# Kernel optimization log

Hardware: AMD Instinct MI355X
Metric: run time of the kernel (lower is better)

Reference implementation:

```python
import jax, jax.numpy as jnp
import numpy as np

N = 100000
D = 16          # input_dim
NUM_FILTERS = 8
NNZ = 1600000


def setup_inputs() -> dict:
    key = jax.random.key(0)
    k1, k2, k3, k4, k5 = jax.random.split(key, 5)
    x = jax.random.normal(k1, (N, D), dtype=jnp.float32)
    L_rows = jax.random.randint(k2, (NNZ,), 0, N, dtype=jnp.int64 if jax.config.jax_enable_x64 else jnp.int32).astype(jnp.int32)
    L_cols = jax.random.randint(k3, (NNZ,), 0, N, dtype=jnp.int32)
    L_v = jax.random.normal(k4, (NNZ,), dtype=jnp.float32)
    node_attr_eig = jax.random.uniform(k5, (N,), dtype=jnp.float32)
    return {"x": x, "L_rows": L_rows, "L_cols": L_cols, "L_v": L_v, "node_attr_eig": node_attr_eig}


def reference(x, L_rows, L_cols, L_v, node_attr_eig):
    n, d = x.shape
    f = NUM_FILTERS
    # exponents = 2 ** arange(num_filters + 1)
    exponents = (2 ** jnp.arange(f + 1)).astype(x.dtype)  # [F+1]
    # coeffs = x.T @ L  ==  (L.T @ x).T ; compute L.T @ x as [N, D]
    # (L.T @ x)[c] = sum over nnz entries (r, c): L_v * x[r]
    LTx = jax.ops.segment_sum(L_v[:, None] * x[L_rows], L_cols, num_segments=n)  # [N, D]
    # exponential eigenfilter bank: w = exp(-eig)^exponents, wavelet differences
    w = jnp.exp(-node_attr_eig)[:, None] ** exponents[None, :]  # [N, F+1]
    w_wav = w[:, :-1] - w[:, 1:]                                # [N, F]
    # g_eig = coeffs[..., None] * w_wav[None, ...] permuted to [N, D, F]
    g_eig = (LTx[:, :, None] * w_wav[:, None, :]).reshape(n, d * f)  # [N, D*F]
    # filtered = L @ g_eig : out[r] = sum over nnz (r, c): L_v * g_eig[c]
    out = jax.ops.segment_sum(L_v[:, None] * g_eig[L_cols], L_rows, num_segments=n)
    return out.reshape(n, d, f)
```

## Files before the change

kernel.cpp:

```cpp
#include <hip/hip_runtime.h>

#define N_NODES   100000
#define D_DIM     16
#define NFILT     8
#define KOUT      128
#define NNZ_CNT   1600000

#define SHIFT1    12
#define NC1       25
#define CAP1      67072
#define NSUB      32
#define CROWS     128
#define NCB       (NC1 * NSUB)
#define CAP       2560
#define EPB       2048
#define NBLKA     ((NNZ_CNT + EPB - 1) / EPB)
#define CHB       ((CAP1 + EPB - 1) / EPB)
#define CPAD      16

__device__ __forceinline__ uint f32_to_bf16_bits(float f) {
    uint u = __float_as_uint(f);
    uint r = (u + 0x7FFFu + ((u >> 16) & 1u)) >> 16;
    return r;
}

__global__ void wav_kernel(const float* __restrict__ eig, ushort* __restrict__ wavb) {
    int n = blockIdx.x * blockDim.x + threadIdx.x;
    if (n >= N_NODES) return;
    float cur = expf(-eig[n]);
    uint pk[4];
#pragma unroll
    for (int h = 0; h < 4; ++h) {
        float nx0 = cur * cur;
        float w0 = cur - nx0;
        float nx1 = nx0 * nx0;
        float w1 = nx0 - nx1;
        cur = nx1;
        pk[h] = f32_to_bf16_bits(w0) | (f32_to_bf16_bits(w1) << 16);
    }
    *(uint4*)(wavb + (size_t)n * NFILT) = make_uint4(pk[0], pk[1], pk[2], pk[3]);
}

__global__ __launch_bounds__(512) void binC_kernel(const int* __restrict__ keys,
                                                   const int* __restrict__ pays,
                                                   const float* __restrict__ v,
                                                   int* __restrict__ gcur1,
                                                   int2* __restrict__ regB) {
    __shared__ int cnt[NC1], offb[NC1], gbase[NC1], cur[NC1];
    __shared__ int2 rec[EPB];
    __shared__ unsigned char rbk[EPB];
    int tid = threadIdx.x;
    int e0 = blockIdx.x * EPB;
    int nE = NNZ_CNT - e0; if (nE > EPB) nE = EPB;

    if (tid < NC1) cnt[tid] = 0;
    __syncthreads();

    int k_[4], p_[4], vb_[4];
    int nk = 0;
#pragma unroll
    for (int kk = 0; kk < 4; ++kk) {
        int i = tid + kk * 512;
        if (i < nE) {
            k_[kk] = keys[e0 + i];
            p_[kk] = pays[e0 + i];
            vb_[kk] = __float_as_int(v[e0 + i]);
            nk = kk + 1;
            atomicAdd(&cnt[k_[kk] >> SHIFT1], 1);
        }
    }
    __syncthreads();

    if (tid == 0) {
        int run = 0;
        for (int b = 0; b < NC1; ++b) { offb[b] = run; run += cnt[b]; }
    }
    if (tid < NC1)
        gbase[tid] = cnt[tid] ? atomicAdd(&gcur1[tid * CPAD], cnt[tid]) : 0;
    __syncthreads();
    if (tid < NC1) cur[tid] = offb[tid];
    __syncthreads();

    for (int kk = 0; kk < nk; ++kk) {
        int b = k_[kk] >> SHIFT1;
        int pos = atomicAdd(&cur[b], 1);
        rec[pos] = make_int2(((k_[kk] & ((1 << SHIFT1) - 1)) << 17) | p_[kk], vb_[kk]);
        rbk[pos] = (unsigned char)b;
    }
    __syncthreads();

    for (int i = tid; i < nE; i += 512) {
        int b = rbk[i];
        int slot = gbase[b] + (i - offb[b]);
        if (slot < CAP1) regB[(size_t)b * CAP1 + slot] = rec[i];
    }
}

__global__ __launch_bounds__(512) void binF_kernel(const int* __restrict__ gcur1,
                                                   const int2* __restrict__ regB,
                                                   int* __restrict__ gcurF,
                                                   int2* __restrict__ regA) {
    __shared__ int cnt[NSUB], offb[NSUB], gbase[NSUB], cur[NSUB];
    __shared__ int2 rec[EPB];
    __shared__ unsigned char rbk[EPB];
    int tid = threadIdx.x;
    int cb = blockIdx.x / CHB;
    int ch = blockIdx.x % CHB;
    int nc = gcur1[cb * CPAD]; if (nc > CAP1) nc = CAP1;
    int cs = ch * EPB;
    if (cs >= nc) return;
    int nE = nc - cs; if (nE > EPB) nE = EPB;
    size_t srcb = (size_t)cb * CAP1 + cs;

    if (tid < NSUB) cnt[tid] = 0;
    __syncthreads();

    int2 my[4]; int msub[4];
    int nk = 0;
#pragma unroll
    for (int kk = 0; kk < 4; ++kk) {
        int i = tid + kk * 512;
        msub[kk] = -1;
        if (i < nE) {
            my[kk] = regB[srcb + i];
            msub[kk] = (my[kk].x >> 24) & (NSUB - 1);
            nk = kk + 1;
            atomicAdd(&cnt[msub[kk]], 1);
        }
    }
    __syncthreads();

    if (tid == 0) {
        int run = 0;
        for (int b = 0; b < NSUB; ++b) { offb[b] = run; run += cnt[b]; }
    }
    if (tid < NSUB)
        gbase[tid] = cnt[tid] ? atomicAdd(&gcurF[(cb * NSUB + tid) * CPAD], cnt[tid]) : 0;
    __syncthreads();
    if (tid < NSUB) cur[tid] = offb[tid];
    __syncthreads();

    for (int kk = 0; kk < nk; ++kk)
        if (msub[kk] >= 0) {
            int pos = atomicAdd(&cur[msub[kk]], 1);
            rec[pos] = make_int2(my[kk].x & 0xFFFFFF, my[kk].y);
            rbk[pos] = (unsigned char)msub[kk];
        }
    __syncthreads();

    for (int i = tid; i < nE; i += 512) {
        int b = rbk[i];
        int slot = gbase[b] + (i - offb[b]);
        if (slot < CAP)
            regA[(size_t)(cb * NSUB + b) * CAP + slot] = rec[i];
    }
}

__global__ __launch_bounds__(512) void sortgather1_kernel(const int* __restrict__ gcurF,
                                                          const int2* __restrict__ regA,
                                                          const float* __restrict__ x,
                                                          uint* __restrict__ LTxP) {
    __shared__ int2 rec[CAP];
    __shared__ int cnt[CROWS];
    __shared__ int sc[CROWS];
    __shared__ int st[CROWS];
    __shared__ int cur[CROWS];
    int tid = threadIdx.x;
    int b = blockIdx.x;
    int nb = gcurF[b * CPAD]; if (nb > CAP) nb = CAP;
    size_t base = (size_t)b * CAP;

    int2 my[5]; int mkey[5];
    if (tid < CROWS) cnt[tid] = 0;
    __syncthreads();
#pragma unroll
    for (int s = 0; s < 5; ++s) {
        int i = tid + s * 512;
        mkey[s] = -1;
        if (i < nb) {
            my[s] = regA[base + i];
            mkey[s] = my[s].x >> 17;
            atomicAdd(&cnt[mkey[s]], 1);
        }
    }
    __syncthreads();

    int cv = (tid < CROWS) ? cnt[tid] : 0;
    if (tid < CROWS) sc[tid] = cv;
    __syncthreads();
    for (int off = 1; off < CROWS; off <<= 1) {
        int t = (tid < CROWS && tid >= off) ? sc[tid - off] : 0;
        __syncthreads();
        if (tid < CROWS) sc[tid] += t;
        __syncthreads();
    }
    if (tid < CROWS) { int s0 = sc[tid] - cv; st[tid] = s0; cur[tid] = s0; }
    __syncthreads();

#pragma unroll
    for (int s = 0; s < 5; ++s)
        if (mkey[s] >= 0) {
            int pos = atomicAdd(&cur[mkey[s]], 1);
            if (pos < CAP) rec[pos] = make_int2(my[s].x & 0x1FFFF, my[s].y);
        }
    __syncthreads();

    int wave = tid >> 6, lane = tid & 63;
    int d = lane & 15, j = lane >> 4;
    for (int cl = wave; cl < CROWS; cl += 8) {
        int c = b * CROWS + cl;
        int i0 = st[cl], e0 = i0 + cnt[cl]; if (e0 > CAP) e0 = CAP;
        float acc = 0.f;
        for (int i = i0 + j; i < e0; i += 4) {
            int2 e = rec[i];
            acc = fmaf(__int_as_float(e.y), x[(size_t)e.x * D_DIM + d], acc);
        }
        acc += __shfl_xor(acc, 16);
        acc += __shfl_xor(acc, 32);
        float hi = __shfl_down(acc, 8);
        if (lane < 8 && c < N_NODES)
            LTxP[(size_t)c * NFILT + lane] =
                f32_to_bf16_bits(acc) | (f32_to_bf16_bits(hi) << 16);
    }
}

__global__ __launch_bounds__(512) void sortgather2_kernel(const int* __restrict__ gcurF,
                                                          const int2* __restrict__ regA,
                                                          const uint* __restrict__ LTxP,
                                                          const ushort* __restrict__ wavb,
                                                          float* __restrict__ out) {
    __shared__ int2 rec[CAP];
    __shared__ int cnt[CROWS];
    __shared__ int sc[CROWS];
    __shared__ int st[CROWS];
    __shared__ int cur[CROWS];
    int tid = threadIdx.x;
    int b = blockIdx.x;
    int nb = gcurF[b * CPAD]; if (nb > CAP) nb = CAP;
    size_t base = (size_t)b * CAP;

    int2 my[5]; int mkey[5];
    if (tid < CROWS) cnt[tid] = 0;
    __syncthreads();
#pragma unroll
    for (int s = 0; s < 5; ++s) {
        int i = tid + s * 512;
        mkey[s] = -1;
        if (i < nb) {
            my[s] = regA[base + i];
            mkey[s] = my[s].x >> 17;
            atomicAdd(&cnt[mkey[s]], 1);
        }
    }
    __syncthreads();

    int cv = (tid < CROWS) ? cnt[tid] : 0;
    if (tid < CROWS) sc[tid] = cv;
    __syncthreads();
    for (int off = 1; off < CROWS; off <<= 1) {
        int t = (tid < CROWS && tid >= off) ? sc[tid - off] : 0;
        __syncthreads();
        if (tid < CROWS) sc[tid] += t;
        __syncthreads();
    }
    if (tid < CROWS) { int s0 = sc[tid] - cv; st[tid] = s0; cur[tid] = s0; }
    __syncthreads();

#pragma unroll
    for (int s = 0; s < 5; ++s)
        if (mkey[s] >= 0) {
            int pos = atomicAdd(&cur[mkey[s]], 1);
            if (pos < CAP) rec[pos] = make_int2(my[s].x & 0x1FFFF, my[s].y);
        }
    __syncthreads();

    int wave = tid >> 6, lane = tid & 63;
    int d0 = lane >> 3;
    int f  = lane & 7;
    for (int rl = wave; rl < CROWS; rl += 8) {
        int row = b * CROWS + rl;
        if (row >= N_NODES) continue;
        int i = st[rl], end = st[rl] + cnt[rl]; if (end > CAP) end = CAP;
        float acc0 = 0.f, acc1 = 0.f;
        for (; i + 4 <= end; i += 4) {
            int2 e0 = rec[i], e1 = rec[i + 1], e2 = rec[i + 2], e3 = rec[i + 3];
            uint l0 = LTxP[e0.x * NFILT + d0];
            uint l1 = LTxP[e1.x * NFILT + d0];
            uint l2 = LTxP[e2.x * NFILT + d0];
            uint l3 = LTxP[e3.x * NFILT + d0];
            uint w0 = wavb[e0.x * NFILT + f];
            uint w1 = wavb[e1.x * NFILT + f];
            uint w2 = wavb[e2.x * NFILT + f];
            uint w3 = wavb[e3.x * NFILT + f];
            float vw0 = __int_as_float(e0.y) * __uint_as_float(w0 << 16);
            float vw1 = __int_as_float(e1.y) * __uint_as_float(w1 << 16);
            float vw2 = __int_as_float(e2.y) * __uint_as_float(w2 << 16);
            float vw3 = __int_as_float(e3.y) * __uint_as_float(w3 << 16);
            acc0 = fmaf(vw0, __uint_as_float(l0 << 16), acc0);
            acc1 = fmaf(vw0, __uint_as_float(l0 & 0xFFFF0000u), acc1);
            acc0 = fmaf(vw1, __uint_as_float(l1 << 16), acc0);
            acc1 = fmaf(vw1, __uint_as_float(l1 & 0xFFFF0000u), acc1);
            acc0 = fmaf(vw2, __uint_as_float(l2 << 16), acc0);
            acc1 = fmaf(vw2, __uint_as_float(l2 & 0xFFFF0000u), acc1);
            acc0 = fmaf(vw3, __uint_as_float(l3 << 16), acc0);
            acc1 = fmaf(vw3, __uint_as_float(l3 & 0xFFFF0000u), acc1);
        }
        for (; i < end; ++i) {
            int2 e = rec[i];
            uint l = LTxP[e.x * NFILT + d0];
            uint w = wavb[e.x * NFILT + f];
            float vw = __int_as_float(e.y) * __uint_as_float(w << 16);
            acc0 = fmaf(vw, __uint_as_float(l << 16), acc0);
            acc1 = fmaf(vw, __uint_as_float(l & 0xFFFF0000u), acc1);
        }
        __builtin_nontemporal_store(acc0, &out[(size_t)row * KOUT + lane]);
        __builtin_nontemporal_store(acc1, &out[(size_t)row * KOUT + 64 + lane]);
    }
}

extern "C" void kernel_launch(void* const* d_in, const int* in_sizes, int n_in,
                              void* d_out, int out_size, void* d_ws, size_t ws_size,
                              hipStream_t stream) {
    const float* x      = (const float*)d_in[0];
    const int*   L_rows = (const int*)  d_in[1];
    const int*   L_cols = (const int*)  d_in[2];
    const float* L_v    = (const float*)d_in[3];
    const float* eig    = (const float*)d_in[4];
    float* out = (float*)d_out;

    uint*   LTxP = (uint*)d_ws;
    ushort* wavb = (ushort*)(LTxP + (size_t)N_NODES * NFILT);
    int2*   regB = (int2*)(wavb + (size_t)N_NODES * NFILT);
    int2*   regA = regB + (size_t)NC1 * CAP1;
    int*    gc1c = (int*)(regA + (size_t)NCB * CAP);
    int*    gc1r = gc1c + NC1 * CPAD;
    int*    gfc  = gc1r + NC1 * CPAD;
    int*    gfr  = gfc + NCB * CPAD;

    hipMemsetAsync(gc1c, 0, (size_t)(2 * NC1 + 2 * NCB) * CPAD * sizeof(int), stream);

    wav_kernel<<<(N_NODES + 255) / 256, 256, 0, stream>>>(eig, wavb);

    binC_kernel<<<NBLKA, 512, 0, stream>>>(L_cols, L_rows, L_v, gc1c, regB);
    binF_kernel<<<NC1 * CHB, 512, 0, stream>>>(gc1c, regB, gfc, regA);
    sortgather1_kernel<<<NCB, 512, 0, stream>>>(gfc, regA, x, LTxP);

    binC_kernel<<<NBLKA, 512, 0, stream>>>(L_rows, L_cols, L_v, gc1r, regB);
    binF_kernel<<<NC1 * CHB, 512, 0, stream>>>(gc1r, regB, gfr, regA);
    sortgather2_kernel<<<NCB, 512, 0, stream>>>(gfr, regA, LTxP, wavb, out);
}
```

Baseline: 277.9 us.

## Fuse both coarse binning passes, interleave LTx with wavelets, use finer row buckets

Merges the two coarse binning launches into one kernel that reads rows, cols and values once and scatters into separate column and row regions, removing a second pass over the COO inputs. LTx and wavelet weights are stored interleaved in one 64-byte record per node, so the second gather touches one cache line per neighbour instead of two. Buckets shrink to 64 rows with 256-thread blocks and a smaller capacity, doubling block count for better load balance. The risks are extra workspace for a second coarse region and a tighter per-bucket capacity that could overflow on skewed inputs.

```diff
diff --git a/kernel.cpp b/kernel.cpp
--- a/kernel.cpp
+++ b/kernel.cpp
@@ -9,22 +9,23 @@
 #define SHIFT1    12
 #define NC1       25
 #define CAP1      67072
-#define NSUB      32
-#define CROWS     128
+#define NSUB      64
+#define CROWS     64
 #define NCB       (NC1 * NSUB)
-#define CAP       2560
+#define CAP       1408
 #define EPB       2048
 #define NBLKA     ((NNZ_CNT + EPB - 1) / EPB)
 #define CHB       ((CAP1 + EPB - 1) / EPB)
 #define CPAD      16
 
+
 __device__ __forceinline__ uint f32_to_bf16_bits(float f) {
     uint u = __float_as_uint(f);
     uint r = (u + 0x7FFFu + ((u >> 16) & 1u)) >> 16;
     return r;
 }
 
-__global__ void wav_kernel(const float* __restrict__ eig, ushort* __restrict__ wavb) {
+__global__ void wav_kernel(const float* __restrict__ eig, uint* __restrict__ combo) {
     int n = blockIdx.x * blockDim.x + threadIdx.x;
     if (n >= N_NODES) return;
     float cur = expf(-eig[n]);
@@ -38,14 +39,16 @@
         cur = nx1;
         pk[h] = f32_to_bf16_bits(w0) | (f32_to_bf16_bits(w1) << 16);
     }
-    *(uint4*)(wavb + (size_t)n * NFILT) = make_uint4(pk[0], pk[1], pk[2], pk[3]);
-}
-
-__global__ __launch_bounds__(512) void binC_kernel(const int* __restrict__ keys,
-                                                   const int* __restrict__ pays,
-                                                   const float* __restrict__ v,
-                                                   int* __restrict__ gcur1,
-                                                   int2* __restrict__ regB) {
+    *(uint4*)(combo + (size_t)n * 16 + 8) = make_uint4(pk[0], pk[1], pk[2], pk[3]);
+}
+
+__global__ __launch_bounds__(512) void binC2_kernel(const int* __restrict__ rows,
+                                                    const int* __restrict__ cols,
+                                                    const float* __restrict__ v,
+                                                    int* __restrict__ gc1c,
+                                                    int* __restrict__ gc1r,
+                                                    int2* __restrict__ regBc,
+                                                    int2* __restrict__ regBr) {
     __shared__ int cnt[NC1], offb[NC1], gbase[NC1], cur[NC1];
     __shared__ int2 rec[EPB];
     __shared__ unsigned char rbk[EPB];
@@ -53,46 +56,66 @@
     int e0 = blockIdx.x * EPB;
     int nE = NNZ_CNT - e0; if (nE > EPB) nE = EPB;
 
-    if (tid < NC1) cnt[tid] = 0;
-    __syncthreads();
-
-    int k_[4], p_[4], vb_[4];
+    int r_[4], c_[4], vb_[4];
     int nk = 0;
 #pragma unroll
     for (int kk = 0; kk < 4; ++kk) {
         int i = tid + kk * 512;
         if (i < nE) {
-            k_[kk] = keys[e0 + i];
-            p_[kk] = pays[e0 + i];
+            r_[kk] = rows[e0 + i];
+            c_[kk] = cols[e0 + i];
             vb_[kk] = __float_as_int(v[e0 + i]);
             nk = kk + 1;
-            atomicAdd(&cnt[k_[kk] >> SHIFT1], 1);
-        }
-    }
-    __syncthreads();
-
-    if (tid == 0) {
-        int run = 0;
-        for (int b = 0; b < NC1; ++b) { offb[b] = run; run += cnt[b]; }
-    }
-    if (tid < NC1)
-        gbase[tid] = cnt[tid] ? atomicAdd(&gcur1[tid * CPAD], cnt[tid]) : 0;
-    __syncthreads();
-    if (tid < NC1) cur[tid] = offb[tid];
-    __syncthreads();
-
+        }
+    }
+
+    if (tid < NC1) cnt[tid] = 0;
+    __syncthreads();
+    for (int kk = 0; kk < nk; ++kk) atomicAdd(&cnt[c_[kk] >> SHIFT1], 1);
+    __syncthreads();
+    if (tid == 0) { int run = 0; for (int b = 0; b < NC1; ++b) { offb[b] = run; run += cnt[b]; } }
+    __syncthreads();
+    if (tid < NC1) {
+        gbase[tid] = cnt[tid] ? atomicAdd(&gc1c[tid * CPAD], cnt[tid]) : 0;
+        cur[tid] = offb[tid];
+    }
+    __syncthreads();
     for (int kk = 0; kk < nk; ++kk) {
-        int b = k_[kk] >> SHIFT1;
+        int b = c_[kk] >> SHIFT1;
         int pos = atomicAdd(&cur[b], 1);
-        rec[pos] = make_int2(((k_[kk] & ((1 << SHIFT1) - 1)) << 17) | p_[kk], vb_[kk]);
+        rec[pos] = make_int2(((c_[kk] & 4095) << 17) | r_[kk], vb_[kk]);
         rbk[pos] = (unsigned char)b;
     }
     __syncthreads();
-
     for (int i = tid; i < nE; i += 512) {
         int b = rbk[i];
         int slot = gbase[b] + (i - offb[b]);
-        if (slot < CAP1) regB[(size_t)b * CAP1 + slot] = rec[i];
+        if (slot < CAP1) regBc[(size_t)b * CAP1 + slot] = rec[i];
+    }
+    __syncthreads();
+
+    if (tid < NC1) cnt[tid] = 0;
+    __syncthreads();
+    for (int kk = 0; kk < nk; ++kk) atomicAdd(&cnt[r_[kk] >> SHIFT1], 1);
+    __syncthreads();
+    if (tid == 0) { int run = 0; for (int b = 0; b < NC1; ++b) { offb[b] = run; run += cnt[b]; } }
+    __syncthreads();
+    if (tid < NC1) {
+        gbase[tid] = cnt[tid] ? atomicAdd(&gc1r[tid * CPAD], cnt[tid]) : 0;
+        cur[tid] = offb[tid];
+    }
+    __syncthreads();
+    for (int kk = 0; kk < nk; ++kk) {
+        int b = r_[kk] >> SHIFT1;
+        int pos = atomicAdd(&cur[b], 1);
+        rec[pos] = make_int2(((r_[kk] & 4095) << 17) | c_[kk], vb_[kk]);
+        rbk[pos] = (unsigned char)b;
+    }
+    __syncthreads();
+    for (int i = tid; i < nE; i += 512) {
+        int b = rbk[i];
+        int slot = gbase[b] + (i - offb[b]);
+        if (slot < CAP1) regBr[(size_t)b * CAP1 + slot] = rec[i];
     }
 }
 
@@ -123,27 +146,25 @@
         msub[kk] = -1;
         if (i < nE) {
             my[kk] = regB[srcb + i];
-            msub[kk] = (my[kk].x >> 24) & (NSUB - 1);
+            msub[kk] = (my[kk].x >> 23) & (NSUB - 1);
             nk = kk + 1;
             atomicAdd(&cnt[msub[kk]], 1);
         }
     }
     __syncthreads();
 
-    if (tid == 0) {
-        int run = 0;
-        for (int b = 0; b < NSUB; ++b) { offb[b] = run; run += cnt[b]; }
-    }
-    if (tid < NSUB)
+    if (tid == 0) { int run = 0; for (int b = 0; b < NSUB; ++b) { offb[b] = run; run += cnt[b]; } }
+    __syncthreads();
+    if (tid < NSUB) {
         gbase[tid] = cnt[tid] ? atomicAdd(&gcurF[(cb * NSUB + tid) * CPAD], cnt[tid]) : 0;
-    __syncthreads();
-    if (tid < NSUB) cur[tid] = offb[tid];
+        cur[tid] = offb[tid];
+    }
     __syncthreads();
 
     for (int kk = 0; kk < nk; ++kk)
         if (msub[kk] >= 0) {
             int pos = atomicAdd(&cur[msub[kk]], 1);
-            rec[pos] = make_int2(my[kk].x & 0xFFFFFF, my[kk].y);
+            rec[pos] = make_int2(my[kk].x & 0x7FFFFF, my[kk].y);
             rbk[pos] = (unsigned char)msub[kk];
         }
     __syncthreads();
@@ -156,26 +177,23 @@
     }
 }
 
-__global__ __launch_bounds__(512) void sortgather1_kernel(const int* __restrict__ gcurF,
+__global__ __launch_bounds__(256) void sortgather1_kernel(const int* __restrict__ gcurF,
                                                           const int2* __restrict__ regA,
                                                           const float* __restrict__ x,
-                                                          uint* __restrict__ LTxP) {
+                                                          uint* __restrict__ combo) {
     __shared__ int2 rec[CAP];
-    __shared__ int cnt[CROWS];
-    __shared__ int sc[CROWS];
-    __shared__ int st[CROWS];
-    __shared__ int cur[CROWS];
+    __shared__ int cnt[CROWS], sc[CROWS], st[CROWS], cur[CROWS];
     int tid = threadIdx.x;
     int b = blockIdx.x;
     int nb = gcurF[b * CPAD]; if (nb > CAP) nb = CAP;
     size_t base = (size_t)b * CAP;
 
-    int2 my[5]; int mkey[5];
+    int2 my[6]; int mkey[6];
     if (tid < CROWS) cnt[tid] = 0;
     __syncthreads();
 #pragma unroll
-    for (int s = 0; s < 5; ++s) {
-        int i = tid + s * 512;
+    for (int s = 0; s < 6; ++s) {
+        int i = tid + s * 256;
         mkey[s] = -1;
         if (i < nb) {
             my[s] = regA[base + i];
@@ -198,7 +216,7 @@
     __syncthreads();
 
 #pragma unroll
-    for (int s = 0; s < 5; ++s)
+    for (int s = 0; s < 6; ++s)
         if (mkey[s] >= 0) {
             int pos = atomicAdd(&cur[mkey[s]], 1);
             if (pos < CAP) rec[pos] = make_int2(my[s].x & 0x1FFFF, my[s].y);
@@ -207,7 +225,7 @@
 
     int wave = tid >> 6, lane = tid & 63;
     int d = lane & 15, j = lane >> 4;
-    for (int cl = wave; cl < CROWS; cl += 8) {
+    for (int cl = wave; cl < CROWS; cl += 4) {
         int c = b * CROWS + cl;
         int i0 = st[cl], e0 = i0 + cnt[cl]; if (e0 > CAP) e0 = CAP;
         float acc = 0.f;
@@ -219,32 +237,28 @@
         acc += __shfl_xor(acc, 32);
         float hi = __shfl_down(acc, 8);
         if (lane < 8 && c < N_NODES)
-            LTxP[(size_t)c * NFILT + lane] =
+            combo[(size_t)c * 16 + lane] =
                 f32_to_bf16_bits(acc) | (f32_to_bf16_bits(hi) << 16);
     }
 }
 
-__global__ __launch_bounds__(512) void sortgather2_kernel(const int* __restrict__ gcurF,
+__global__ __launch_bounds__(256) void sortgather2_kernel(const int* __restrict__ gcurF,
                                                           const int2* __restrict__ regA,
-                                                          const uint* __restrict__ LTxP,
-                                                          const ushort* __restrict__ wavb,
+                                                          const uint* __restrict__ combo,
                                                           float* __restrict__ out) {
     __shared__ int2 rec[CAP];
-    __shared__ int cnt[CROWS];
-    __shared__ int sc[CROWS];
-    __shared__ int st[CROWS];
-    __shared__ int cur[CROWS];
+    __shared__ int cnt[CROWS], sc[CROWS], st[CROWS], cur[CROWS];
     int tid = threadIdx.x;
     int b = blockIdx.x;
     int nb = gcurF[b * CPAD]; if (nb > CAP) nb = CAP;
     size_t base = (size_t)b * CAP;
 
-    int2 my[5]; int mkey[5];
+    int2 my[6]; int mkey[6];
     if (tid < CROWS) cnt[tid] = 0;
     __syncthreads();
 #pragma unroll
-    for (int s = 0; s < 5; ++s) {
-        int i = tid + s * 512;
+    for (int s = 0; s < 6; ++s) {
+        int i = tid + s * 256;
         mkey[s] = -1;
         if (i < nb) {
             my[s] = regA[base + i];
@@ -267,7 +281,7 @@
     __syncthreads();
 
 #pragma unroll
-    for (int s = 0; s < 5; ++s)
+    for (int s = 0; s < 6; ++s)
         if (mkey[s] >= 0) {
             int pos = atomicAdd(&cur[mkey[s]], 1);
             if (pos < CAP) rec[pos] = make_int2(my[s].x & 0x1FFFF, my[s].y);
@@ -277,21 +291,21 @@
     int wave = tid >> 6, lane = tid & 63;
     int d0 = lane >> 3;
     int f  = lane & 7;
-    for (int rl = wave; rl < CROWS; rl += 8) {
+    for (int rl = wave; rl < CROWS; rl += 4) {
         int row = b * CROWS + rl;
         if (row >= N_NODES) continue;
         int i = st[rl], end = st[rl] + cnt[rl]; if (end > CAP) end = CAP;
         float acc0 = 0.f, acc1 = 0.f;
         for (; i + 4 <= end; i += 4) {
             int2 e0 = rec[i], e1 = rec[i + 1], e2 = rec[i + 2], e3 = rec[i + 3];
-            uint l0 = LTxP[e0.x * NFILT + d0];
-            uint l1 = LTxP[e1.x * NFILT + d0];
-            uint l2 = LTxP[e2.x * NFILT + d0];
-            uint l3 = LTxP[e3.x * NFILT + d0];
-            uint w0 = wavb[e0.x * NFILT + f];
-            uint w1 = wavb[e1.x * NFILT + f];
-            uint w2 = wavb[e2.x * NFILT + f];
-            uint w3 = wavb[e3.x * NFILT + f];
+            uint l0 = combo[(size_t)e0.x * 16 + d0];
+            uint l1 = combo[(size_t)e1.x * 16 + d0];
+            uint l2 = combo[(size_t)e2.x * 16 + d0];
+            uint l3 = combo[(size_t)e3.x * 16 + d0];
+            uint w0 = ((const ushort*)(combo + (size_t)e0.x * 16 + 8))[f];
+            uint w1 = ((const ushort*)(combo + (size_t)e1.x * 16 + 8))[f];
+            uint w2 = ((const ushort*)(combo + (size_t)e2.x * 16 + 8))[f];
+            uint w3 = ((const ushort*)(combo + (size_t)e3.x * 16 + 8))[f];
             float vw0 = __int_as_float(e0.y) * __uint_as_float(w0 << 16);
             float vw1 = __int_as_float(e1.y) * __uint_as_float(w1 << 16);
             float vw2 = __int_as_float(e2.y) * __uint_as_float(w2 << 16);
@@ -307,8 +321,8 @@
         }
         for (; i < end; ++i) {
             int2 e = rec[i];
-            uint l = LTxP[e.x * NFILT + d0];
-            uint w = wavb[e.x * NFILT + f];
+            uint l = combo[(size_t)e.x * 16 + d0];
+            uint w = ((const ushort*)(combo + (size_t)e.x * 16 + 8))[f];
             float vw = __int_as_float(e.y) * __uint_as_float(w << 16);
             acc0 = fmaf(vw, __uint_as_float(l << 16), acc0);
             acc1 = fmaf(vw, __uint_as_float(l & 0xFFFF0000u), acc1);
@@ -328,24 +342,24 @@
     const float* eig    = (const float*)d_in[4];
     float* out = (float*)d_out;
 
-    uint*   LTxP = (uint*)d_ws;
-    ushort* wavb = (ushort*)(LTxP + (size_t)N_NODES * NFILT);
-    int2*   regB = (int2*)(wavb + (size_t)N_NODES * NFILT);
-    int2*   regA = regB + (size_t)NC1 * CAP1;
-    int*    gc1c = (int*)(regA + (size_t)NCB * CAP);
-    int*    gc1r = gc1c + NC1 * CPAD;
-    int*    gfc  = gc1r + NC1 * CPAD;
-    int*    gfr  = gfc + NCB * CPAD;
+    uint* combo = (uint*)d_ws;
+    int2* regBc = (int2*)(combo + (size_t)N_NODES * 16);
+    int2* regBr = regBc + (size_t)NC1 * CAP1;
+    int2* regA  = regBr + (size_t)NC1 * CAP1;
+    int*  gc1c  = (int*)(regA + (size_t)NCB * CAP);
+    int*  gc1r  = gc1c + NC1 * CPAD;
+    int*  gfc   = gc1r + NC1 * CPAD;
+    int*  gfr   = gfc + NCB * CPAD;
 
     hipMemsetAsync(gc1c, 0, (size_t)(2 * NC1 + 2 * NCB) * CPAD * sizeof(int), stream);
 
-    wav_kernel<<<(N_NODES + 255) / 256, 256, 0, stream>>>(eig, wavb);
-
-    binC_kernel<<<NBLKA, 512, 0, stream>>>(L_cols, L_rows, L_v, gc1c, regB);
-    binF_kernel<<<NC1 * CHB, 512, 0, stream>>>(gc1c, regB, gfc, regA);
-    sortgather1_kernel<<<NCB, 512, 0, stream>>>(gfc, regA, x, LTxP);
-
-    binC_kernel<<<NBLKA, 512, 0, stream>>>(L_rows, L_cols, L_v, gc1r, regB);
-    binF_kernel<<<NC1 * CHB, 512, 0, stream>>>(gc1r, regB, gfr, regA);
-    sortgather2_kernel<<<NCB, 512, 0, stream>>>(gfr, regA, LTxP, wavb, out);
-}
+    wav_kernel<<<(N_NODES + 255) / 256, 256, 0, stream>>>(eig, combo);
+
+    binC2_kernel<<<NBLKA, 512, 0, stream>>>(L_rows, L_cols, L_v, gc1c, gc1r, regBc, regBr);
+
+    binF_kernel<<<NC1 * CHB, 512, 0, stream>>>(gc1c, regBc, gfc, regA);
+    sortgather1_kernel<<<NCB, 256, 0, stream>>>(gfc, regA, x, combo);
+
+    binF_kernel<<<NC1 * CHB, 512, 0, stream>>>(gc1r, regBr, gfr, regA);
+    sortgather2_kernel<<<NCB, 256, 0, stream>>>(gfr, regA, combo, out);
+}
```

Measured after the change: 260.0 us. 6.4% less time.
